# Performance work log

Hardware: AMD Instinct MI355X
Metric: run time of the kernel (lower is better)

Reference implementation:

```python
import jax, jax.numpy as jnp
import numpy as np
import math

N_EMBD = 1024
N_HEAD_DIM = 64
B, S = 8, 2048

def setup_inputs() -> dict:
    key = jax.random.key(0)
    ks = jax.random.split(key, 8)
    x = jax.random.normal(ks[0], (B, S, N_EMBD), dtype=jnp.float32)
    padding_mask = jax.random.randint(ks[1], (B, S), 0, 2).astype(jnp.bool_)
    scale = 1.0 / math.sqrt(N_EMBD)
    Wq = jax.random.normal(ks[2], (N_HEAD_DIM, N_EMBD), dtype=jnp.float32) * scale
    bq = jnp.zeros((N_HEAD_DIM,), dtype=jnp.float32)
    Wk = jax.random.normal(ks[3], (N_HEAD_DIM, N_EMBD), dtype=jnp.float32) * scale
    bk = jnp.zeros((N_HEAD_DIM,), dtype=jnp.float32)
    Wv = jax.random.normal(ks[4], (N_HEAD_DIM, N_EMBD), dtype=jnp.float32) * scale
    bv = jnp.zeros((N_HEAD_DIM,), dtype=jnp.float32)
    return {"x": x, "Wq": Wq, "bq": bq, "Wk": Wk, "bk": bk, "Wv": Wv, "bv": bv,
            "padding_mask": padding_mask}

def reference(x, Wq, bq, Wk, bk, Wv, bv, padding_mask):
    # q,k,v: [B,S,D] via Linear (x @ W^T + b)
    q = jnp.einsum('bse,de->bsd', x, Wq) + bq
    k = jnp.einsum('bse,de->bsd', x, Wk) + bk
    v = jnp.einsum('bse,de->bsd', x, Wv) + bv
    scale = 1.0 / math.sqrt(k.shape[-1])
    att = jnp.einsum('bqd,bkd->bqk', q, k) * scale  # [B,S,S]
    # padding_mask [B,S] -> [B,1,S]: True positions masked to -inf
    att = jnp.where(padding_mask[:, None, :], -jnp.inf, att)
    att = jax.nn.softmax(att, axis=-1)
    # attn_dropout omitted (eval mode / identity)
    return jnp.einsum('bqk,bkd->bqd', att, v)
```

## Files before the change

### kernel.cpp

```cpp
#include <hip/hip_runtime.h>
#include <hip/hip_bf16.h>

#define B_ 8
#define S_ 2048
#define E_ 1024
#define D_ 64
#define VT_STRIDE 2112

typedef short short8 __attribute__((ext_vector_type(8)));
typedef short short4v __attribute__((ext_vector_type(4)));
typedef float floatx4 __attribute__((ext_vector_type(4)));

static __device__ __forceinline__ short bf16_bits(float f) {
    __hip_bfloat16 h = __float2bfloat16(f);
    return *reinterpret_cast<short*>(&h);
}
static __device__ __forceinline__ float bits_to_f(short s) {
    __hip_bfloat16 h = *reinterpret_cast<__hip_bfloat16*>(&s);
    return __bfloat162float(h);
}
static __device__ __forceinline__ void split8(const float* __restrict__ p,
                                              short8& hi, short8& lo) {
    #pragma unroll
    for (int j = 0; j < 8; j++) {
        float f = p[j];
        short h = bf16_bits(f);
        hi[j] = h;
        lo[j] = bf16_bits(f - bits_to_f(h));
    }
}
static __device__ __forceinline__ void split8v(const float v[8],
                                               short8& hi, short8& lo) {
    #pragma unroll
    for (int j = 0; j < 8; j++) {
        float f = v[j];
        short h = bf16_bits(f);
        hi[j] = h;
        lo[j] = bf16_bits(f - bits_to_f(h));
    }
}
static __device__ __forceinline__ void dma16(const void* src, void* lds_dst) {
    __builtin_amdgcn_global_load_lds(
        (const __attribute__((address_space(1))) unsigned int*)src,
        (__attribute__((address_space(3))) unsigned int*)lds_dst, 16, 0, 0);
}

__global__ __launch_bounds__(256) void prep_kernel(
    const float* __restrict__ Wq, const float* __restrict__ Wk,
    const float* __restrict__ Wv, short8* __restrict__ Wpk8,
    const void* __restrict__ mask_raw, float* __restrict__ maskf,
    float* __restrict__ maskc, short* __restrict__ cidx,
    int* __restrict__ nrounds, short* __restrict__ Khi,
    short* __restrict__ Vt)
{
    __shared__ unsigned int red[256];
    if (blockIdx.x < 96) {
        const int t = blockIdx.x * 256 + threadIdx.x;
        const int l16  = t & 15;
        const int quad = (t >> 4) & 3;
        const int nb   = (t >> 6) & 3;
        const int m    = (t >> 8) % 3;
        const int e0c  = (t >> 8) / 3;
        const float* W = (m == 0) ? Wq : ((m == 1) ? Wk : Wv);
        short8 hi, lo;
        split8(W + (size_t)(nb * 16 + l16) * E_ + e0c * 32 + quad * 8, hi, lo);
        Wpk8[(size_t)e0c * 768 + m * 256 + nb * 64 + quad * 16 + l16] = hi;
    } else {
        const unsigned int* w = (const unsigned int*)mask_raw;
        unsigned int local = 0;
        for (int i = threadIdx.x; i < 4096; i += 256) local |= w[i];
        red[threadIdx.x] = local;
        __syncthreads();
        for (int s = 128; s > 0; s >>= 1) {
            if (threadIdx.x < s) red[threadIdx.x] |= red[threadIdx.x + s];
            __syncthreads();
        }
        const unsigned int ov = red[0];
        const bool is_u8 = (ov > 1u) && ((ov >> 24) <= 1u);
        if (blockIdx.x < 160) {
            const int i = (blockIdx.x - 96) * 256 + threadIdx.x;
            int v;
            if (ov == 0u)      v = 0;
            else if (is_u8)    v = (int)((const unsigned char*)mask_raw)[i];
            else               v = (((const unsigned int*)mask_raw)[i] != 0u);
            maskf[i] = v ? -1e30f : 0.0f;
        } else {
            const int b = blockIdx.x - 160;
            int um[8];
            #pragma unroll
            for (int j = 0; j < 8; j++) {
                const int i = b * 2048 + (int)threadIdx.x * 8 + j;
                int v;
                if (ov == 0u)      v = 0;
                else if (is_u8)    v = (int)((const unsigned char*)mask_raw)[i];
                else               v = (w[i] != 0u);
                um[j] = v ? 0 : 1;
            }
            int cnt = 0;
            #pragma unroll
            for (int j = 0; j < 8; j++) cnt += um[j];
            __syncthreads();
            red[threadIdx.x] = (unsigned int)cnt;
            __syncthreads();
            for (int off = 1; off < 256; off <<= 1) {
                unsigned int a = 0;
                if ((int)threadIdx.x >= off) a = red[threadIdx.x - off];
                __syncthreads();
                red[threadIdx.x] += a;
                __syncthreads();
            }
            const int total = (int)red[255];
            int pos = (int)red[threadIdx.x] - cnt;
            #pragma unroll
            for (int j = 0; j < 8; j++) {
                const int s = (int)threadIdx.x * 8 + j;
                cidx[b * 2048 + s] = (short)(um[j] ? pos : -1);
                pos += um[j];
            }
            int nr = (total + 127) >> 7;
            if (nr == 0) nr = 1;
            if (threadIdx.x == 0) nrounds[b] = nr;
            for (int k = threadIdx.x; k < 2048; k += 256)
                maskc[b * 2048 + k] = (k < total) ? 0.0f : -1e30f;
            const int nkpad = nr * 128;
            const int padn = (nkpad - total) * 64;
            for (int idx = threadIdx.x; idx < padn; idx += 256) {
                const int p = total + (idx >> 6);
                const int d = idx & 63;
                Khi[((size_t)b * 2048 + p) * 64 + d] = 0;
                Vt[((size_t)(b * 64 + d)) * VT_STRIDE + p] = 0;
            }
        }
    }
}

__global__ __launch_bounds__(512, 4) void qkv_kernel(
    const float* __restrict__ x, const short8* __restrict__ Wpk8,
    const float* __restrict__ bq, const float* __restrict__ bk,
    const float* __restrict__ bv,
    const float* __restrict__ maskf, const short* __restrict__ cidx,
    short* __restrict__ Qhi, short* __restrict__ Qlo,
    short* __restrict__ Khi, short* __restrict__ Vt)
{
    __shared__ alignas(16) float  xs[2][2][1024];
    __shared__ alignas(16) short8 wt[2][1536];
    const int tid  = threadIdx.x;
    const int wave = tid >> 6;
    const int nb   = wave & 3;
    const int rt   = wave >> 2;
    const int lane = tid & 63;
    const int l16  = lane & 15;
    const int quad = lane >> 4;
    const int row0 = blockIdx.x * 32;

    const int xr_  = (tid >> 3) & 31;
    const int xc_  = tid >> 8;
    const float* xsrc = x + (size_t)(row0 + xr_) * E_ + xc_ * 32 +
                        (((tid & 7) ^ (xr_ & 7)) * 4);
    const int xdst = xc_ * 1024 + xr_ * 32 + (tid & 7) * 4;

    floatx4 acc[3];
    #pragma unroll
    for (int m = 0; m < 3; m++) acc[m] = (floatx4){0.f,0.f,0.f,0.f};

    #pragma unroll
    for (int i = 0; i < 3; i++)
        dma16(Wpk8 + (size_t)i * 512 + tid, &wt[0][i * 512 + tid]);
    dma16(xsrc, &xs[0][0][0] + xdst);

    int buf = 0;
    for (int R = 0; R < 16; ++R) {
        __syncthreads();
        if (R + 1 < 16) {
            #pragma unroll
            for (int i = 0; i < 3; i++)
                dma16(Wpk8 + (size_t)(R + 1) * 1536 + i * 512 + tid,
                      &wt[buf ^ 1][i * 512 + tid]);
            dma16(xsrc + (R + 1) * 64, &xs[buf ^ 1][0][0] + xdst);
        }

        #pragma unroll
        for (int c = 0; c < 2; c++) {
            const int rr = rt * 16 + l16;
            const int rx = rr & 7;
            const float* xrp = &xs[buf][c][rr * 32];
            float4 a0 = *reinterpret_cast<const float4*>(xrp + (((2 * quad)     ^ rx) * 4));
            float4 a1 = *reinterpret_cast<const float4*>(xrp + (((2 * quad + 1) ^ rx) * 4));
            float av[8] = {a0.x, a0.y, a0.z, a0.w, a1.x, a1.y, a1.z, a1.w};
            short8 ah, al;
            split8v(av, ah, al);
            #pragma unroll
            for (int m = 0; m < 3; m++) {
                short8 wh = wt[buf][c * 768 + m * 256 + nb * 64 + lane];
                acc[m] = __builtin_amdgcn_mfma_f32_16x16x32_bf16(al, wh, acc[m], 0, 0, 0);
                acc[m] = __builtin_amdgcn_mfma_f32_16x16x32_bf16(ah, wh, acc[m], 0, 0, 0);
            }
        }
        buf ^= 1;
    }

    const int d = nb * 16 + l16;
    const float bqv = bq[d];
    const float bkv = bk[d];
    const float bvv = bv[d];
    const int bch = row0 >> 11;
    const int rowbase = row0 + rt * 16 + quad * 4;
    #pragma unroll
    for (int r = 0; r < 4; r++) {
        const size_t row = (size_t)(rowbase + r);
        const float q = (acc[0][r] + bqv) * 0.125f;
        const short qhv = bf16_bits(q);
        Qhi[row * 64 + d] = qhv;
        Qlo[row * 64 + d] = bf16_bits(q - bits_to_f(qhv));
        if (maskf[row] == 0.0f) {
            const int cpos = (int)cidx[row];
            Khi[((size_t)(bch << 11) + cpos) * 64 + d] = bf16_bits(acc[1][r] + bkv);
            Vt[((size_t)(bch * 64 + d)) * VT_STRIDE + cpos] = bf16_bits(acc[2][r] + bvv);
        }
    }
}

union alignas(16) AttnLds {
    struct { short8 kts[4][512]; short8 vts[4][512]; } st;
    struct {
        float Osh[4][16][65];
        float msh[4][16], lsh[4][16];
    } mg;
};

__global__ __launch_bounds__(256, 2) void attn_kernel(
    const short* __restrict__ Qhi, const short* __restrict__ Qlo,
    const short* __restrict__ Khi, const short* __restrict__ Vt,
    const float* __restrict__ maskc, const int* __restrict__ nrounds,
    float* __restrict__ out)
{
    __shared__ AttnLds lds;
    __shared__ short PlT[4][16][72];

    const int tid  = threadIdx.x;
    const int wave = tid >> 6;
    const int qsub = wave & 1;
    const int par  = wave >> 1;
    const int lane = tid & 63;
    const int l16  = lane & 15;
    const int quad = lane >> 4;
    const int b    = blockIdx.x >> 6;
    const int qt   = blockIdx.x & 63;
    const int NR   = nrounds[b];
    const size_t qbase  = (size_t)b * S_ + qt * 32 + qsub * 16;
    const size_t kplane = (size_t)b * S_;
    const short* Vb = Vt + (size_t)b * 64 * VT_STRIDE;

    short8 qh[2], ql[2];
    #pragma unroll
    for (int dc = 0; dc < 2; dc++) {
        qh[dc] = *reinterpret_cast<const short8*>(Qhi + (qbase + l16) * 64 + dc * 32 + quad * 8);
        ql[dc] = *reinterpret_cast<const short8*>(Qlo + (qbase + l16) * 64 + dc * 32 + quad * 8);
    }

    float m = -1e30f, l = 0.f;
    floatx4 O[4];
    #pragma unroll
    for (int ob = 0; ob < 4; ob++) O[ob] = (floatx4){0.f,0.f,0.f,0.f};

    #pragma unroll
    for (int p = 0; p < 2; p++) {
        #pragma unroll
        for (int i = 0; i < 2; i++) {
            const int c = i * 256 + tid;
            const int r = c >> 3, cs = c & 7;
            dma16(Khi + (kplane + p * 64 + r) * 64 + ((cs ^ (r & 7)) * 8),
                  &lds.st.kts[p][c]);
            dma16(Vb + (size_t)r * VT_STRIDE + p * 64 + ((cs ^ (r & 7)) * 8),
                  &lds.st.vts[p][c]);
        }
    }
    float4 mk4[4];
    #pragma unroll
    for (int kb = 0; kb < 4; kb++)
        mk4[kb] = *reinterpret_cast<const float4*>(
            maskc + kplane + par * 64 + kb * 16 + quad * 4);

    for (int R = 0; R < NR; ++R) {
        __syncthreads();
        const int set = R & 1;
        if (R + 1 < NR) {
            const int nset = set ^ 1;
            const int kt2 = (R + 1) * 128;
            #pragma unroll
            for (int p = 0; p < 2; p++) {
                #pragma unroll
                for (int i = 0; i < 2; i++) {
                    const int c = i * 256 + tid;
                    const int r = c >> 3, cs = c & 7;
                    dma16(Khi + (kplane + kt2 + p * 64 + r) * 64 + ((cs ^ (r & 7)) * 8),
                          &lds.st.kts[nset * 2 + p][c]);
                    dma16(Vb + (size_t)r * VT_STRIDE + kt2 + p * 64 + ((cs ^ (r & 7)) * 8),
                          &lds.st.vts[nset * 2 + p][c]);
                }
            }
        }
        const int buf = set * 2 + par;

        floatx4 sc[4];
        #pragma unroll
        for (int kb = 0; kb < 4; kb++) {
            floatx4 a = (floatx4){0.f,0.f,0.f,0.f};
            #pragma unroll
            for (int kc = 0; kc < 2; kc++) {
                const int key = kb * 16 + l16;
                short8 kf = lds.st.kts[buf][key * 8 + ((kc * 4 + quad) ^ (key & 7))];
                a = __builtin_amdgcn_mfma_f32_16x16x32_bf16(kf, qh[kc], a, 0, 0, 0);
                a = __builtin_amdgcn_mfma_f32_16x16x32_bf16(kf, ql[kc], a, 0, 0, 0);
            }
            sc[kb] = a;
        }
        #pragma unroll
        for (int kb = 0; kb < 4; kb++) {
            const float* mkp = reinterpret_cast<const float*>(&mk4[kb]);
            #pragma unroll
            for (int r = 0; r < 4; r++) sc[kb][r] += mkp[r];
        }

        if (R + 1 < NR) {
            const int ktn = (R + 1) * 128 + par * 64;
            #pragma unroll
            for (int kb = 0; kb < 4; kb++)
                mk4[kb] = *reinterpret_cast<const float4*>(
                    maskc + kplane + ktn + kb * 16 + quad * 4);
        }

        float mx = -1e30f;
        #pragma unroll
        for (int kb = 0; kb < 4; kb++)
            #pragma unroll
            for (int r = 0; r < 4; r++) mx = fmaxf(mx, sc[kb][r]);
        mx = fmaxf(mx, __shfl_xor(mx, 16, 64));
        mx = fmaxf(mx, __shfl_xor(mx, 32, 64));
        const float mnew  = fmaxf(fmaxf(m, mx), -1e29f);
        const float alpha = __expf(m - mnew);
        float ps = 0.f;
        #pragma unroll
        for (int kb = 0; kb < 4; kb++)
            #pragma unroll
            for (int r = 0; r < 4; r++) {
                const float pe = __expf(sc[kb][r] - mnew);
                sc[kb][r] = pe;
                ps += pe;
            }
        ps += __shfl_xor(ps, 16, 64);
        ps += __shfl_xor(ps, 32, 64);
        l = l * alpha + ps;
        m = mnew;
        #pragma unroll
        for (int ob = 0; ob < 4; ob++) O[ob] *= alpha;

        #pragma unroll
        for (int kb = 0; kb < 4; kb++)
            #pragma unroll
            for (int r = 0; r < 4; r++)
                PlT[wave][l16][kb * 16 + quad * 4 + r] = bf16_bits(sc[kb][r]);
        short8 pf[2];
        #pragma unroll
        for (int kc = 0; kc < 2; kc++)
            pf[kc] = *reinterpret_cast<const short8*>(&PlT[wave][l16][kc * 32 + quad * 8]);

        #pragma unroll
        for (int ob = 0; ob < 4; ob++)
            #pragma unroll
            for (int kc = 0; kc < 2; kc++) {
                const int dd = ob * 16 + l16;
                short8 vf = lds.st.vts[buf][dd * 8 + ((kc * 4 + quad) ^ (dd & 7))];
                O[ob] = __builtin_amdgcn_mfma_f32_16x16x32_bf16(vf, pf[kc], O[ob], 0, 0, 0);
            }
    }

    __syncthreads();
    #pragma unroll
    for (int ob = 0; ob < 4; ob++)
        #pragma unroll
        for (int r = 0; r < 4; r++)
            lds.mg.Osh[wave][l16][ob * 16 + quad * 4 + r] = O[ob][r];
    if (quad == 0) {
        lds.mg.msh[wave][l16] = m;
        lds.mg.lsh[wave][l16] = l;
    }
    __syncthreads();

    #pragma unroll
    for (int part = 0; part < 8; part++) {
        const int idx = part * 256 + tid;
        const int q = idx >> 6;
        const int d = idx & 63;
        const int w0 = (q >> 4), qq = q & 15;
        const float m0 = lds.mg.msh[w0][qq], m1 = lds.mg.msh[w0 + 2][qq];
        const float ms = fmaxf(m0, m1);
        const float x0 = __expf(m0 - ms), x1 = __expf(m1 - ms);
        const float lt = lds.mg.lsh[w0][qq] * x0 + lds.mg.lsh[w0 + 2][qq] * x1;
        const float oa = lds.mg.Osh[w0][qq][d] * x0 + lds.mg.Osh[w0 + 2][qq][d] * x1;
        out[((size_t)b * S_ + qt * 32 + q) * 64 + d] = oa / lt;
    }
}

extern "C" void kernel_launch(void* const* d_in, const int* in_sizes, int n_in,
                              void* d_out, int out_size, void* d_ws, size_t ws_size,
                              hipStream_t stream) {
    const float* x  = (const float*)d_in[0];
    const float* Wq = (const float*)d_in[1];
    const float* bq = (const float*)d_in[2];
    const float* Wk = (const float*)d_in[3];
    const float* bk = (const float*)d_in[4];
    const float* Wv = (const float*)d_in[5];
    const float* bv = (const float*)d_in[6];
    const void* mask = d_in[7];

    char* ws = (char*)d_ws;
    const size_t PLANE = (size_t)B_ * S_ * D_;
    short* Wpk = (short*)ws;
    short* Qhi = (short*)(ws + 768 * 1024);
    short* Qlo = Qhi + PLANE;
    short* Khi = Qlo + PLANE;
    short* Vt  = Khi + PLANE;
    float* maskf = (float*)(Vt + (size_t)512 * VT_STRIDE);
    float* maskc = maskf + 16384;
    short* cidx  = (short*)(maskc + 16384);
    int*   nround = (int*)(cidx + 16384);

    prep_kernel<<<168, 256, 0, stream>>>(Wq, Wk, Wv, (short8*)Wpk, mask, maskf,
                                         maskc, cidx, nround, Khi, Vt);
    qkv_kernel<<<512, 512, 0, stream>>>(x, (const short8*)Wpk, bq, bk, bv,
                                        maskf, cidx, Qhi, Qlo, Khi, Vt);
    attn_kernel<<<512, 256, 0, stream>>>(Qhi, Qlo, Khi, Vt, maskc, nround,
                                         (float*)d_out);
}
```

Baseline: 152.7 us.

## Fuse prep, QKV and attention kernels into one cooperative kernel with grid syncs

Merges the three separate launches (weight/mask prep, QKV projection, flash-style attention) into a single cooperative kernel that uses grid.sync between phases. Shared memory is overlaid in a union across phases. The aim is to remove two kernel launch gaps and inter-kernel drain/fill. In exchange, the attention phase runs with only half the threads of each 512-thread block, grid syncs add barrier cost, and occupancy is constrained by the cooperative launch and the combined LDS footprint. The old three-kernel path stays as a fallback if the cooperative launch fails.

Result: slower. 473.1 us (+209.9%).

```diff
diff --git a/kernel.cpp b/kernel.cpp
--- a/kernel.cpp
+++ b/kernel.cpp
@@ -1,5 +1,8 @@
 #include <hip/hip_runtime.h>
+#include <hip/hip_cooperative_groups.h>
 #include <hip/hip_bf16.h>
+
+namespace cg = cooperative_groups;
 
 #define B_ 8
 #define S_ 2048
@@ -43,6 +46,361 @@
     __builtin_amdgcn_global_load_lds(
         (const __attribute__((address_space(1))) unsigned int*)src,
         (__attribute__((address_space(3))) unsigned int*)lds_dst, 16, 0, 0);
+}
+
+union alignas(16) FusedLds {
+    unsigned int red[512];
+    struct { float xs[2][2][1024]; short8 wt[2][1536]; } qk;
+    struct {
+        union {
+            struct { short8 kts[4][512]; short8 vts[4][512]; } st;
+            struct { float Osh[4][16][65]; float msh[4][16], lsh[4][16]; } mg;
+        } u;
+        short PlT[4][16][72];
+    } at;
+};
+
+__global__ __launch_bounds__(512, 4) void fused_kernel(
+    const float* __restrict__ x,
+    const float* __restrict__ Wq, const float* __restrict__ bq,
+    const float* __restrict__ Wk, const float* __restrict__ bk,
+    const float* __restrict__ Wv, const float* __restrict__ bv,
+    const void* __restrict__ mask_raw,
+    short8* __restrict__ Wpk8,
+    short* __restrict__ Qhi, short* __restrict__ Qlo,
+    short* __restrict__ Khi, short* __restrict__ Vt,
+    float* __restrict__ maskf, float* __restrict__ maskc,
+    short* __restrict__ cidx, int* __restrict__ nrounds,
+    float* __restrict__ out)
+{
+    __shared__ FusedLds L;
+    cg::grid_group grid = cg::this_grid();
+    const int tid = threadIdx.x;
+    const int bx  = blockIdx.x;
+
+    if (bx < 48) {
+        const int t = bx * 512 + tid;
+        const int l16  = t & 15;
+        const int quad = (t >> 4) & 3;
+        const int nb   = (t >> 6) & 3;
+        const int m    = (t >> 8) % 3;
+        const int e0c  = (t >> 8) / 3;
+        const float* W = (m == 0) ? Wq : ((m == 1) ? Wk : Wv);
+        short8 hi, lo;
+        split8(W + (size_t)(nb * 16 + l16) * E_ + e0c * 32 + quad * 8, hi, lo);
+        Wpk8[(size_t)e0c * 768 + m * 256 + nb * 64 + quad * 16 + l16] = hi;
+    } else if (bx < 88) {
+        const unsigned int* w = (const unsigned int*)mask_raw;
+        unsigned int local = 0;
+        for (int i = tid; i < 4096; i += 512) local |= w[i];
+        L.red[tid] = local;
+        __syncthreads();
+        for (int s = 256; s > 0; s >>= 1) {
+            if (tid < s) L.red[tid] |= L.red[tid + s];
+            __syncthreads();
+        }
+        const unsigned int ov = L.red[0];
+        const bool is_u8 = (ov > 1u) && ((ov >> 24) <= 1u);
+        if (bx < 80) {
+            const int i = (bx - 48) * 512 + tid;
+            int v;
+            if (ov == 0u)      v = 0;
+            else if (is_u8)    v = (int)((const unsigned char*)mask_raw)[i];
+            else               v = (w[i] != 0u);
+            maskf[i] = v ? -1e30f : 0.0f;
+        } else {
+            const int b = bx - 80;
+            int um[4];
+            #pragma unroll
+            for (int j = 0; j < 4; j++) {
+                const int i = b * 2048 + tid * 4 + j;
+                int v;
+                if (ov == 0u)      v = 0;
+                else if (is_u8)    v = (int)((const unsigned char*)mask_raw)[i];
+                else               v = (w[i] != 0u);
+                um[j] = v ? 0 : 1;
+            }
+            const int cnt = um[0] + um[1] + um[2] + um[3];
+            __syncthreads();
+            L.red[tid] = (unsigned int)cnt;
+            __syncthreads();
+            for (int off = 1; off < 512; off <<= 1) {
+                unsigned int a = 0;
+                if (tid >= off) a = L.red[tid - off];
+                __syncthreads();
+                L.red[tid] += a;
+                __syncthreads();
+            }
+            const int total = (int)L.red[511];
+            int pos = (int)L.red[tid] - cnt;
+            #pragma unroll
+            for (int j = 0; j < 4; j++) {
+                cidx[b * 2048 + tid * 4 + j] = (short)(um[j] ? pos : -1);
+                pos += um[j];
+            }
+            int nr = (total + 127) >> 7;
+            if (nr == 0) nr = 1;
+            if (tid == 0) nrounds[b] = nr;
+            for (int k = tid; k < 2048; k += 512)
+                maskc[b * 2048 + k] = (k < total) ? 0.0f : -1e30f;
+            const int padn = (nr * 128 - total) * 64;
+            for (int idx = tid; idx < padn; idx += 512) {
+                const int p = total + (idx >> 6);
+                const int d = idx & 63;
+                Khi[((size_t)b * 2048 + p) * 64 + d] = 0;
+                Vt[((size_t)(b * 64 + d)) * VT_STRIDE + p] = 0;
+            }
+        }
+    }
+
+    __threadfence();
+    grid.sync();
+
+    {
+        const int wave = tid >> 6;
+        const int nb   = wave & 3;
+        const int rt   = wave >> 2;
+        const int lane = tid & 63;
+        const int l16  = lane & 15;
+        const int quad = lane >> 4;
+        const int row0 = bx * 32;
+
+        const int xr_  = (tid >> 3) & 31;
+        const int xc_  = tid >> 8;
+        const float* xsrc = x + (size_t)(row0 + xr_) * E_ + xc_ * 32 +
+                            (((tid & 7) ^ (xr_ & 7)) * 4);
+        const int xdst = xc_ * 1024 + xr_ * 32 + (tid & 7) * 4;
+
+        floatx4 acc[3];
+        #pragma unroll
+        for (int m = 0; m < 3; m++) acc[m] = (floatx4){0.f,0.f,0.f,0.f};
+
+        #pragma unroll
+        for (int i = 0; i < 3; i++)
+            dma16(Wpk8 + (size_t)i * 512 + tid, &L.qk.wt[0][i * 512 + tid]);
+        dma16(xsrc, &L.qk.xs[0][0][0] + xdst);
+
+        int buf = 0;
+        for (int R = 0; R < 16; ++R) {
+            __syncthreads();
+            if (R + 1 < 16) {
+                #pragma unroll
+                for (int i = 0; i < 3; i++)
+                    dma16(Wpk8 + (size_t)(R + 1) * 1536 + i * 512 + tid,
+                          &L.qk.wt[buf ^ 1][i * 512 + tid]);
+                dma16(xsrc + (R + 1) * 64, &L.qk.xs[buf ^ 1][0][0] + xdst);
+            }
+
+            #pragma unroll
+            for (int c = 0; c < 2; c++) {
+                const int rr = rt * 16 + l16;
+                const int rx = rr & 7;
+                const float* xrp = &L.qk.xs[buf][c][rr * 32];
+                float4 a0 = *reinterpret_cast<const float4*>(xrp + (((2 * quad)     ^ rx) * 4));
+                float4 a1 = *reinterpret_cast<const float4*>(xrp + (((2 * quad + 1) ^ rx) * 4));
+                float av[8] = {a0.x, a0.y, a0.z, a0.w, a1.x, a1.y, a1.z, a1.w};
+                short8 ah, al;
+                split8v(av, ah, al);
+                #pragma unroll
+                for (int m = 0; m < 3; m++) {
+                    short8 wh = L.qk.wt[buf][c * 768 + m * 256 + nb * 64 + lane];
+                    acc[m] = __builtin_amdgcn_mfma_f32_16x16x32_bf16(al, wh, acc[m], 0, 0, 0);
+                    acc[m] = __builtin_amdgcn_mfma_f32_16x16x32_bf16(ah, wh, acc[m], 0, 0, 0);
+                }
+            }
+            buf ^= 1;
+        }
+
+        const int d = nb * 16 + l16;
+        const float bqv = bq[d];
+        const float bkv = bk[d];
+        const float bvv = bv[d];
+        const int bch = row0 >> 11;
+        const int rowbase = row0 + rt * 16 + quad * 4;
+        #pragma unroll
+        for (int r = 0; r < 4; r++) {
+            const size_t row = (size_t)(rowbase + r);
+            const float q = (acc[0][r] + bqv) * 0.125f;
+            const short qhv = bf16_bits(q);
+            Qhi[row * 64 + d] = qhv;
+            Qlo[row * 64 + d] = bf16_bits(q - bits_to_f(qhv));
+            if (maskf[row] == 0.0f) {
+                const int cpos = (int)cidx[row];
+                Khi[((size_t)(bch << 11) + cpos) * 64 + d] = bf16_bits(acc[1][r] + bkv);
+                Vt[((size_t)(bch * 64 + d)) * VT_STRIDE + cpos] = bf16_bits(acc[2][r] + bvv);
+            }
+        }
+    }
+
+    __threadfence();
+    grid.sync();
+
+    if (tid >= 256) return;
+    {
+        const int t    = tid;
+        const int wave = t >> 6;
+        const int qsub = wave & 1;
+        const int par  = wave >> 1;
+        const int lane = t & 63;
+        const int l16  = lane & 15;
+        const int quad = lane >> 4;
+        const int b    = bx >> 6;
+        const int qt   = bx & 63;
+        const int NR   = nrounds[b];
+        const size_t qbase  = (size_t)b * S_ + qt * 32 + qsub * 16;
+        const size_t kplane = (size_t)b * S_;
+        const short* Vb = Vt + (size_t)b * 64 * VT_STRIDE;
+
+        short8 qh[2], ql[2];
+        #pragma unroll
+        for (int dc = 0; dc < 2; dc++) {
+            qh[dc] = *reinterpret_cast<const short8*>(Qhi + (qbase + l16) * 64 + dc * 32 + quad * 8);
+            ql[dc] = *reinterpret_cast<const short8*>(Qlo + (qbase + l16) * 64 + dc * 32 + quad * 8);
+        }
+
+        float m = -1e30f, l = 0.f;
+        floatx4 O[4];
+        #pragma unroll
+        for (int ob = 0; ob < 4; ob++) O[ob] = (floatx4){0.f,0.f,0.f,0.f};
+
+        #pragma unroll
+        for (int p = 0; p < 2; p++) {
+            #pragma unroll
+            for (int i = 0; i < 2; i++) {
+                const int c = i * 256 + t;
+                const int r = c >> 3, cs = c & 7;
+                dma16(Khi + (kplane + p * 64 + r) * 64 + ((cs ^ (r & 7)) * 8),
+                      &L.at.u.st.kts[p][c]);
+                dma16(Vb + (size_t)r * VT_STRIDE + p * 64 + ((cs ^ (r & 7)) * 8),
+                      &L.at.u.st.vts[p][c]);
+            }
+        }
+        float4 mk4[4];
+        #pragma unroll
+        for (int kb = 0; kb < 4; kb++)
+            mk4[kb] = *reinterpret_cast<const float4*>(
+                maskc + kplane + par * 64 + kb * 16 + quad * 4);
+
+        for (int R = 0; R < NR; ++R) {
+            __syncthreads();
+            const int set = R & 1;
+            if (R + 1 < NR) {
+                const int nset = set ^ 1;
+                const int kt2 = (R + 1) * 128;
+                #pragma unroll
+                for (int p = 0; p < 2; p++) {
+                    #pragma unroll
+                    for (int i = 0; i < 2; i++) {
+                        const int c = i * 256 + t;
+                        const int r = c >> 3, cs = c & 7;
+                        dma16(Khi + (kplane + kt2 + p * 64 + r) * 64 + ((cs ^ (r & 7)) * 8),
+                              &L.at.u.st.kts[nset * 2 + p][c]);
+                        dma16(Vb + (size_t)r * VT_STRIDE + kt2 + p * 64 + ((cs ^ (r & 7)) * 8),
+                              &L.at.u.st.vts[nset * 2 + p][c]);
+                    }
+                }
+            }
+            const int buf = set * 2 + par;
+
+            floatx4 sc[4];
+            #pragma unroll
+            for (int kb = 0; kb < 4; kb++) {
+                floatx4 a = (floatx4){0.f,0.f,0.f,0.f};
+                #pragma unroll
+                for (int kc = 0; kc < 2; kc++) {
+                    const int key = kb * 16 + l16;
+                    short8 kf = L.at.u.st.kts[buf][key * 8 + ((kc * 4 + quad) ^ (key & 7))];
+                    a = __builtin_amdgcn_mfma_f32_16x16x32_bf16(kf, qh[kc], a, 0, 0, 0);
+                    a = __builtin_amdgcn_mfma_f32_16x16x32_bf16(kf, ql[kc], a, 0, 0, 0);
+                }
+                sc[kb] = a;
+            }
+            #pragma unroll
+            for (int kb = 0; kb < 4; kb++) {
+                const float* mkp = reinterpret_cast<const float*>(&mk4[kb]);
+                #pragma unroll
+                for (int r = 0; r < 4; r++) sc[kb][r] += mkp[r];
+            }
+
+            if (R + 1 < NR) {
+                const int ktn = (R + 1) * 128 + par * 64;
+                #pragma unroll
+                for (int kb = 0; kb < 4; kb++)
+                    mk4[kb] = *reinterpret_cast<const float4*>(
+                        maskc + kplane + ktn + kb * 16 + quad * 4);
+            }
+
+            float mx = -1e30f;
+            #pragma unroll
+            for (int kb = 0; kb < 4; kb++)
+                #pragma unroll
+                for (int r = 0; r < 4; r++) mx = fmaxf(mx, sc[kb][r]);
+            mx = fmaxf(mx, __shfl_xor(mx, 16, 64));
+            mx = fmaxf(mx, __shfl_xor(mx, 32, 64));
+            const float mnew  = fmaxf(fmaxf(m, mx), -1e29f);
+            const float alpha = __expf(m - mnew);
+            float ps = 0.f;
+            #pragma unroll
+            for (int kb = 0; kb < 4; kb++)
+                #pragma unroll
+                for (int r = 0; r < 4; r++) {
+                    const float pe = __expf(sc[kb][r] - mnew);
+                    sc[kb][r] = pe;
+                    ps += pe;
+                }
+            ps += __shfl_xor(ps, 16, 64);
+            ps += __shfl_xor(ps, 32, 64);
+            l = l * alpha + ps;
+            m = mnew;
+            #pragma unroll
+            for (int ob = 0; ob < 4; ob++) O[ob] *= alpha;
+
+            #pragma unroll
+            for (int kb = 0; kb < 4; kb++)
+                #pragma unroll
+                for (int r = 0; r < 4; r++)
+                    L.at.PlT[wave][l16][kb * 16 + quad * 4 + r] = bf16_bits(sc[kb][r]);
+            short8 pf[2];
+            #pragma unroll
+            for (int kc = 0; kc < 2; kc++)
+                pf[kc] = *reinterpret_cast<const short8*>(&L.at.PlT[wave][l16][kc * 32 + quad * 8]);
+
+            #pragma unroll
+            for (int ob = 0; ob < 4; ob++)
+                #pragma unroll
+                for (int kc = 0; kc < 2; kc++) {
+                    const int dd = ob * 16 + l16;
+                    short8 vf = L.at.u.st.vts[buf][dd * 8 + ((kc * 4 + quad) ^ (dd & 7))];
+                    O[ob] = __builtin_amdgcn_mfma_f32_16x16x32_bf16(vf, pf[kc], O[ob], 0, 0, 0);
+                }
+        }
+
+        __syncthreads();
+        #pragma unroll
+        for (int ob = 0; ob < 4; ob++)
+            #pragma unroll
+            for (int r = 0; r < 4; r++)
+                L.at.u.mg.Osh[wave][l16][ob * 16 + quad * 4 + r] = O[ob][r];
+        if (quad == 0) {
+            L.at.u.mg.msh[wave][l16] = m;
+            L.at.u.mg.lsh[wave][l16] = l;
+        }
+        __syncthreads();
+
+        #pragma unroll
+        for (int part = 0; part < 8; part++) {
+            const int idx = part * 256 + t;
+            const int q = idx >> 6;
+            const int d = idx & 63;
+            const int w0 = (q >> 4), qq = q & 15;
+            const float m0 = L.at.u.mg.msh[w0][qq], m1 = L.at.u.mg.msh[w0 + 2][qq];
+            const float ms = fmaxf(m0, m1);
+            const float x0 = __expf(m0 - ms), x1 = __expf(m1 - ms);
+            const float lt = L.at.u.mg.lsh[w0][qq] * x0 + L.at.u.mg.lsh[w0 + 2][qq] * x1;
+            const float oa = L.at.u.mg.Osh[w0][qq][d] * x0 + L.at.u.mg.Osh[w0 + 2][qq][d] * x1;
+            out[((size_t)b * S_ + qt * 32 + q) * 64 + d] = oa / lt;
+        }
+    }
 }
 
 __global__ __launch_bounds__(256) void prep_kernel(
@@ -122,8 +480,7 @@
             if (threadIdx.x == 0) nrounds[b] = nr;
             for (int k = threadIdx.x; k < 2048; k += 256)
                 maskc[b * 2048 + k] = (k < total) ? 0.0f : -1e30f;
-            const int nkpad = nr * 128;
-            const int padn = (nkpad - total) * 64;
+            const int padn = (nr * 128 - total) * 64;
             for (int idx = threadIdx.x; idx < padn; idx += 256) {
                 const int p = total + (idx >> 6);
                 const int d = idx & 63;
@@ -178,7 +535,6 @@
                       &wt[buf ^ 1][i * 512 + tid]);
             dma16(xsrc + (R + 1) * 64, &xs[buf ^ 1][0][0] + xdst);
         }
-
         #pragma unroll
         for (int c = 0; c < 2; c++) {
             const int rr = rt * 16 + l16;
@@ -416,7 +772,7 @@
 
     char* ws = (char*)d_ws;
     const size_t PLANE = (size_t)B_ * S_ * D_;
-    short* Wpk = (short*)ws;
+    short8* Wpk8 = (short8*)ws;
     short* Qhi = (short*)(ws + 768 * 1024);
     short* Qlo = Qhi + PLANE;
     short* Khi = Qlo + PLANE;
@@ -425,11 +781,24 @@
     float* maskc = maskf + 16384;
     short* cidx  = (short*)(maskc + 16384);
     int*   nround = (int*)(cidx + 16384);
-
-    prep_kernel<<<168, 256, 0, stream>>>(Wq, Wk, Wv, (short8*)Wpk, mask, maskf,
-                                         maskc, cidx, nround, Khi, Vt);
-    qkv_kernel<<<512, 512, 0, stream>>>(x, (const short8*)Wpk, bq, bk, bv,
-                                        maskf, cidx, Qhi, Qlo, Khi, Vt);
-    attn_kernel<<<512, 256, 0, stream>>>(Qhi, Qlo, Khi, Vt, maskc, nround,
-                                         (float*)d_out);
-}
+    float* outp = (float*)d_out;
+
+    void* args[] = {
+        (void*)&x, (void*)&Wq, (void*)&bq, (void*)&Wk, (void*)&bk,
+        (void*)&Wv, (void*)&bv, (void*)&mask,
+        (void*)&Wpk8, (void*)&Qhi, (void*)&Qlo, (void*)&Khi, (void*)&Vt,
+        (void*)&maskf, (void*)&maskc, (void*)&cidx, (void*)&nround,
+        (void*)&outp
+    };
+    hipError_t e = hipLaunchCooperativeKernel((void*)fused_kernel,
+                                              dim3(512), dim3(512),
+                                              args, 0, stream);
+    if (e != hipSuccess) {
+        prep_kernel<<<168, 256, 0, stream>>>(Wq, Wk, Wv, (short8*)Wpk8, mask,
+                                             maskf, maskc, cidx, nround, Khi, Vt);
+        qkv_kernel<<<512, 512, 0, stream>>>(x, (const short8*)Wpk8, bq, bk, bv,
+                                            maskf, cidx, Qhi, Qlo, Khi, Vt);
+        attn_kernel<<<512, 256, 0, stream>>>(Qhi, Qlo, Khi, Vt, maskc, nround,
+                                             (float*)d_out);
+    }
+}
```
